# Optimization experiments

Measured on AMD Instinct MI355X. Metric: run time of the kernel, lower is better.

## Reference

```python
import jax, jax.numpy as jnp
import numpy as np
from jax import lax

B, S, D, T = 64, 256, 1024, 60
HIST = 20  # last-20 window of attn / decoder-state history


def setup_inputs() -> dict:
    key = jax.random.key(0)
    ks = jax.random.split(key, 8)
    e_outputs = jax.random.normal(ks[0], (B, S, D), jnp.float32)
    queries = jax.random.normal(ks[1], (B, T, D), jnp.float32)
    # attention weights over source frames: rows sum to 1
    attns = jax.nn.softmax(jax.random.normal(ks[2], (B, T, S), jnp.float32), axis=-1)
    g = 0.02
    Wr = jax.random.normal(ks[3], (D, 1), jnp.float32) * g
    br = jnp.zeros((1,), jnp.float32)
    Wa = jax.random.normal(ks[4], (D, 1), jnp.float32) * g
    ba = jnp.zeros((1,), jnp.float32)
    Wq = jax.random.normal(ks[5], (D, D), jnp.float32) / np.sqrt(D)
    Wn = jax.random.normal(ks[6], (2 * D, 1), jnp.float32) * g
    bn = jnp.zeros((1,), jnp.float32)
    return {"e_outputs": e_outputs, "queries": queries, "attns": attns,
            "Wr": Wr, "br": br, "Wa": Wa, "ba": ba, "Wq": Wq, "Wn": Wn, "bn": bn}


def reference(e_outputs, queries, attns, Wr, br, Wa, ba, Wq, Wn, bn):
    Bn, Sn, Dn = e_outputs.shape
    # decay1[i] = (i+1)/20 ; decay2[i] = 1-(i+1)/50, zero-padded past 50 frames
    decay1 = (jnp.arange(HIST, dtype=jnp.float32) + 1.0) / 20.0
    idx = jnp.arange(Sn, dtype=jnp.float32)
    add0 = jnp.where(idx < 50, 1.0 - (idx + 1.0) / 50.0, 0.0)
    add_state0 = add0[None, :, None]                       # [1,S,1]
    mem0 = e_outputs * add_state0                          # [B,S,D]
    abuf0 = jnp.zeros((HIST, Bn, Sn), e_outputs.dtype)
    qbuf0 = jnp.zeros((HIST, Bn, Dn), e_outputs.dtype)

    def step(carry, x):
        mem, add_state, abuf, qbuf, i = carry
        attn_i, q_i = x                                    # [B,S], [B,D]
        # read: selected frame before memory update
        sel = jnp.einsum('bs,bsd->bd', attn_i, mem)
        # roll history buffers (newest at slot HIST-1)
        abuf = jnp.concatenate([abuf[1:], attn_i[None]], axis=0)
        qbuf = jnp.concatenate([qbuf[1:], q_i[None]], axis=0)
        k = jnp.minimum(i + 1, HIST)
        valid = jnp.arange(HIST) >= (HIST - k)
        temp = jax.nn.softmax(jnp.where(valid, decay1, -jnp.inf))
        attn_w = jnp.einsum('t,tbs->bs', temp, abuf)       # decayed attn sum
        query_s = jnp.einsum('t,tbd->bd', temp, qbuf)      # decayed query sum
        remove_prob = jax.nn.sigmoid(q_i @ Wr + br)[:, :, None]   # [B,1,1]
        add_prob = jax.nn.sigmoid(q_i @ Wa + ba)[:, :, None]      # [B,1,1]
        sim = jax.nn.sigmoid(jnp.einsum('bsd,bd->bs', mem, query_s @ Wq))[..., None]
        mem = mem * (1.0 - remove_prob * attn_w[..., None] * sim)
        last_ctx = jnp.einsum('bs,bsd->bd', attn_w, e_outputs)[:, None, :]
        cat = jnp.concatenate([e_outputs, jnp.broadcast_to(last_ctx, e_outputs.shape)], axis=-1)
        nxt = jax.nn.sigmoid(cat @ Wn + bn)                # [B,S,1]
        mem = mem + e_outputs * (1.0 - add_state) * (add_prob * nxt)
        add_state = add_state + (1.0 - add_state) * (add_prob * nxt)
        return (mem, add_state, abuf, qbuf, i + 1), sel

    init = (mem0, jnp.broadcast_to(add_state0, (Bn, Sn, 1)), abuf0, qbuf0, jnp.int32(0))
    xs = (attns.transpose(1, 0, 2), queries.transpose(1, 0, 2))
    _, sels = lax.scan(step, init, xs)
    return sels.transpose(1, 0, 2)                         # [B,T,D]
```

## Files before the change

### kernel.cpp

```cpp
#include <hip/hip_runtime.h>
#include <math.h>


#define Bn 64
#define Sn 256
#define Dn 1024
#define Tn 60
#define HISTn 20
#define LDK 72
#define K05 1.0512710963760241f
#define EINV 0.36787944117144233f
#define LOG2E 1.4426950408889634f

typedef __bf16 bf16x8 __attribute__((ext_vector_type(8)));
typedef float f32x4 __attribute__((ext_vector_type(4)));
typedef unsigned short us8 __attribute__((ext_vector_type(8)));

typedef const __attribute__((address_space(1))) unsigned int* gas_u32p;
typedef __attribute__((address_space(3))) unsigned int* las_u32p;

__device__ __forceinline__ void gl16(const unsigned short* g, unsigned short* l){
  __builtin_amdgcn_global_load_lds((gas_u32p)g, (las_u32p)l, 16, 0, 0);
}

__device__ __forceinline__ unsigned short f2bf(float f){
  unsigned int x; __builtin_memcpy(&x,&f,4);
  unsigned int lsb = (x >> 16) & 1u;
  x += 0x7fffu + lsb;
  return (unsigned short)(x >> 16);
}
__device__ __forceinline__ float sigmoidf_(float x){
  float e = __builtin_amdgcn_exp2f(-x * LOG2E);
  return __builtin_amdgcn_rcpf(1.0f + e);
}

__global__ __launch_bounds__(256) void convQW(
    const float* __restrict__ Q, const float* __restrict__ Wr,
    const float* __restrict__ br, const float* __restrict__ Wa,
    const float* __restrict__ ba, const float* __restrict__ Wq,
    float* __restrict__ rp, float* __restrict__ ap,
    unsigned short* __restrict__ Qbf, unsigned short* __restrict__ WT)
{
  int tid = threadIdx.x;
  int bx = blockIdx.x;
  if (bx < Bn*Tn){
    int row = bx;
    float4 x = ((const float4*)(Q + (size_t)row*Dn))[tid];
    float4 a = ((const float4*)Wr)[tid];
    float4 b = ((const float4*)Wa)[tid];
    unsigned short o[4] = {f2bf(x.x), f2bf(x.y), f2bf(x.z), f2bf(x.w)};
    *(uint2*)&Qbf[(size_t)row*Dn + tid*4] = *(uint2*)o;
    float s1 = x.x*a.x + x.y*a.y + x.z*a.z + x.w*a.w;
    float s2 = x.x*b.x + x.y*b.y + x.z*b.z + x.w*b.w;
    for (int off = 32; off; off >>= 1){
      s1 += __shfl_down(s1, off, 64);
      s2 += __shfl_down(s2, off, 64);
    }
    __shared__ float r1[4], r2[4];
    int lane = tid & 63, wv = tid >> 6;
    if (lane == 0){ r1[wv] = s1; r2[wv] = s2; }
    __syncthreads();
    if (tid == 0){
      rp[row] = sigmoidf_(r1[0]+r1[1]+r1[2]+r1[3] + br[0]);
      ap[row] = sigmoidf_(r2[0]+r2[1]+r2[2]+r2[3] + ba[0]);
    }
  } else {
    __shared__ __align__(16) unsigned short Tt[64][LDK];
    int t = bx - Bn*Tn;
    int n0 = (t >> 4)*64, k0 = (t & 15)*64;
    int kl = tid >> 4, nl4 = (tid & 15)*4;
    #pragma unroll
    for (int it = 0; it < 4; it++){
      int k = kl + it*16;
      float4 v = *(const float4*)&Wq[(size_t)(k0+k)*Dn + n0 + nl4];
      Tt[nl4+0][k] = f2bf(v.x); Tt[nl4+1][k] = f2bf(v.y);
      Tt[nl4+2][k] = f2bf(v.z); Tt[nl4+3][k] = f2bf(v.w);
    }
    __syncthreads();
    int nr = tid >> 2, kg = (tid & 3)*16;
    *(us8*)&WT[(size_t)(n0+nr)*Dn + k0+kg]   = *(us8*)&Tt[nr][kg];
    *(us8*)&WT[(size_t)(n0+nr)*Dn + k0+kg+8] = *(us8*)&Tt[nr][kg+8];
  }
}

__global__ __launch_bounds__(256) void qw_e(
    const unsigned short* __restrict__ Qbf,
    const unsigned short* __restrict__ WT,
    const float* __restrict__ E, const float* __restrict__ Wn,
    unsigned short* __restrict__ QWbf,
    unsigned short* __restrict__ Ebf,
    float* __restrict__ eW1, float* __restrict__ eW2)
{
  int tid = threadIdx.x;
  if (blockIdx.x < (Bn*Tn/64)*(Dn/64)){
    __shared__ __align__(16) unsigned short As0_[64*64], Bs0_[64*64];
    __shared__ __align__(16) unsigned short As1_[64*64], Bs1_[64*64];
    int bx = (blockIdx.x & 7)*120 + (blockIdx.x >> 3);
    int m0 = (bx >> 4) * 64, n0 = (bx & 15) * 64;
    int lane = tid & 63, wave = tid >> 6;
    int quad = lane >> 4, l16 = lane & 15;
    f32x4 acc[4];
    #pragma unroll
    for (int nt=0;nt<4;nt++)
      #pragma unroll
      for (int r=0;r<4;r++) acc[nt][r]=0.f;
    int c0 = wave*2;
    int srow = c0*8 + (lane >> 3);
    int scol = ((lane & 7) ^ (lane >> 3)) * 8;
    const unsigned short* gA0 = Qbf + (size_t)(m0 + srow)*Dn + scol;
    const unsigned short* gA1 = gA0 + 8*Dn;
    const unsigned short* gB0 = WT  + (size_t)(n0 + srow)*Dn + scol;
    const unsigned short* gB1 = gB0 + 8*Dn;
    int mrow = wave*16 + l16;

    #define STAGE_QW(K, A_, B_) { \
      gl16(gA0 + (K), &A_[c0*512]);       \
      gl16(gA1 + (K), &A_[c0*512 + 512]); \
      gl16(gB0 + (K), &B_[c0*512]);       \
      gl16(gB1 + (K), &B_[c0*512 + 512]); }
    #define COMP_QW(A_, B_) { \
      _Pragma("unroll") \
      for (int kk = 0; kk < 2; kk++){ \
        bf16x8 a = *(const bf16x8*)&A_[ mrow*64 + ((kk*32 + quad*8) ^ ((mrow&7)*8)) ]; \
        _Pragma("unroll") \
        for (int nt=0;nt<4;nt++){ \
          int nrow = nt*16 + l16; \
          bf16x8 bb = *(const bf16x8*)&B_[ nrow*64 + ((kk*32 + quad*8) ^ ((nrow&7)*8)) ]; \
          acc[nt] = __builtin_amdgcn_mfma_f32_16x16x32_bf16(a, bb, acc[nt], 0, 0, 0); \
        } \
      } }

    STAGE_QW(0, As0_, Bs0_);
    __syncthreads();
    #pragma unroll
    for (int k0 = 0; k0 < Dn; k0 += 128){
      STAGE_QW(k0+64, As1_, Bs1_);
      COMP_QW(As0_, Bs0_);
      __syncthreads();
      if (k0+128 < Dn) STAGE_QW(k0+128, As0_, Bs0_);
      COMP_QW(As1_, Bs1_);
      __syncthreads();
    }
    #undef STAGE_QW
    #undef COMP_QW

    #pragma unroll
    for (int nt=0;nt<4;nt++)
      #pragma unroll
      for (int r=0;r<4;r++){
        int m = m0 + wave*16 + quad*4 + r;
        int n = n0 + nt*16 + l16;
        QWbf[(size_t)m*Dn + n] = f2bf(acc[nt][r]);
      }
  } else {
    int row = (blockIdx.x - (Bn*Tn/64)*(Dn/64))*4 + (tid >> 6);
    int lane = tid & 63;
    const float* er = E + (size_t)row*Dn;
    unsigned short* ebr = Ebf + (size_t)row*Dn;
    float d1 = 0.f, d2 = 0.f;
    #pragma unroll
    for (int c = 0; c < 4; c++){
      int idx = c*64 + lane;
      float4 v = ((const float4*)er)[idx];
      float4 w1 = ((const float4*)Wn)[idx];
      float4 w2 = ((const float4*)(Wn + Dn))[idx];
      unsigned short o[4] = {f2bf(v.x), f2bf(v.y), f2bf(v.z), f2bf(v.w)};
      ((uint2*)ebr)[idx] = *(uint2*)o;
      d1 += v.x*w1.x + v.y*w1.y + v.z*w1.z + v.w*w1.w;
      d2 += v.x*w2.x + v.y*w2.y + v.z*w2.z + v.w*w2.w;
    }
    #pragma unroll
    for (int off = 32; off; off >>= 1){
      d1 += __shfl_down(d1, off, 64);
      d2 += __shfl_down(d2, off, 64);
    }
    if (lane == 0){ eW1[row] = d1; eW2[row] = d2; }
  }
}

__global__ __launch_bounds__(256) void g_scan(
    const unsigned short* __restrict__ QWbf,
    const unsigned short* __restrict__ Ebf,
    const float* __restrict__ At,
    const float* __restrict__ rp,
    const float* __restrict__ ap,
    const float* __restrict__ eW1,
    const float* __restrict__ eW2,
    const float* __restrict__ bnp,
    unsigned short* __restrict__ Pbf)
{
  __shared__ __align__(16) unsigned short As0_[64][LDK], As1_[64][LDK];
  __shared__ __align__(16) unsigned short Bs0_[32][LDK], Bs1_[32][LDK];
  __shared__ __align__(16) float AtL[Tn][32], GL[Tn][32];
  __shared__ float Rsh[Tn], lcs[Tn], rps[Tn], aps[Tn], invd[Tn];
  int b = blockIdx.x, s0 = blockIdx.y * 32;
  int tid = threadIdx.x, lane = tid & 63, wave = tid >> 6;
  int quad = lane >> 4, l16 = lane & 15;

  {
    float4 e2v = ((const float4*)(eW2 + (size_t)b*Sn))[lane];
    const float* at_b = At + (size_t)b*Tn*Sn;
    #pragma unroll
    for (int w = 0; w < 15; w++){
      int j = wave + w*4;
      float4 a4 = ((const float4*)(at_b + (size_t)j*Sn))[lane];
      float v = a4.x*e2v.x + a4.y*e2v.y + a4.z*e2v.z + a4.w*e2v.w;
      #pragma unroll
      for (int off = 32; off; off >>= 1) v += __shfl_down(v, off, 64);
      if (lane == 0) Rsh[j] = v;
    }
  }
  {
    const float* at_c = At + (size_t)b*Tn*Sn + s0;
    #pragma unroll
    for (int it = 0; it < 2; it++){
      int idx = it*256 + tid;
      int r = idx >> 3, c4 = (idx & 7)*4;
      if (r < Tn) *(float4*)&AtL[r][c4] = *(const float4*)&at_c[(size_t)r*Sn + c4];
    }
  }
  if (tid < Tn){
    rps[tid] = rp[b*Tn + tid];
    aps[tid] = ap[b*Tn + tid];
  }

  f32x4 acc[2];
  #pragma unroll
  for (int nt=0;nt<2;nt++)
    #pragma unroll
    for (int r=0;r<4;r++) acc[nt][r]=0.f;
  int sr = tid >> 2, sk = (tid & 3)*16;
  int brw = tid >> 3, bk = (tid & 7)*8;
  const unsigned short* aRow = QWbf + ((size_t)(b*Tn + sr))*Dn;
  const unsigned short* bRow = Ebf  + ((size_t)(b*Sn + s0 + brw))*Dn;

  #define LOADR(K, ra0, ra1, rb0) { \
    if (sr < Tn){ ra0 = *(const us8*)&aRow[(K)+sk]; ra1 = *(const us8*)&aRow[(K)+sk+8]; } \
    else { ra0 = (us8)0; ra1 = (us8)0; } \
    rb0 = *(const us8*)&bRow[(K)+bk]; }
  #define STORER(A_, B_, ra0, ra1, rb0) { \
    *(us8*)&A_[sr][sk]   = ra0; *(us8*)&A_[sr][sk+8] = ra1; \
    *(us8*)&B_[brw][bk]  = rb0; }
  #define COMP_G(A_, B_) { \
    _Pragma("unroll") \
    for (int kk = 0; kk < 64; kk += 32){ \
      bf16x8 a = *(const bf16x8*)&A_[wave*16 + l16][kk + quad*8]; \
      _Pragma("unroll") \
      for (int nt=0;nt<2;nt++){ \
        bf16x8 bb = *(const bf16x8*)&B_[nt*16 + l16][kk + quad*8]; \
        acc[nt] = __builtin_amdgcn_mfma_f32_16x16x32_bf16(a, bb, acc[nt], 0, 0, 0); \
      } \
    } }

  us8 pa0, pa1, pb0, qa0, qa1, qb0;
  LOADR(0, pa0, pa1, pb0);
  STORER(As0_, Bs0_, pa0, pa1, pb0);
  for (int k0 = 0; k0 < Dn; k0 += 128){
    LOADR(k0+64, qa0, qa1, qb0);
    __syncthreads();
    COMP_G(As0_, Bs0_);
    STORER(As1_, Bs1_, qa0, qa1, qb0);
    if (k0+128 < Dn) LOADR(k0+128, pa0, pa1, pb0);
    __syncthreads();
    COMP_G(As1_, Bs1_);
    if (k0+128 < Dn) STORER(As0_, Bs0_, pa0, pa1, pb0);
  }
  #undef LOADR
  #undef STORER
  #undef COMP_G

  #pragma unroll
  for (int nt=0;nt<2;nt++)
    #pragma unroll
    for (int r=0;r<4;r++){
      int t = wave*16 + quad*4 + r;
      if (t < Tn) GL[t][nt*16 + l16] = acc[nt][r];
    }
  __syncthreads();

  if (tid < Tn){
    int i = tid;
    int j0 = (i - HISTn + 1 > 0) ? i - HISTn + 1 : 0;
    float num = 0.f, den = 0.f, wj = 1.f;
    #pragma unroll 1
    for (int j = 0; j <= i; j++){
      wj *= K05;
      if (j >= j0){ num += wj * Rsh[j]; den += wj; }
    }
    float inv = __builtin_amdgcn_rcpf(den);
    lcs[i] = num * inv;
    invd[i] = inv;
  }
  __syncthreads();

  if (tid < 32){
    int s = s0 + tid;
    float M = (s < 50) ? (1.0f - (s+1)/50.0f) : 0.0f;
    float A = M;
    float bnv = bnp[0];
    float e1 = eW1[b*Sn + s];
    unsigned short* P_b = Pbf + (size_t)b*Tn*Sn + s;
    float num_a = 0.f, num_q = 0.f, wi = 1.f;
    float a_new = AtL[0][tid], g_new = GL[0][tid];
    #pragma unroll 1
    for (int i = 0; i < Tn; i++){
      float a_nx = 0.f, g_nx = 0.f;
      if (i+1 < Tn){ a_nx = AtL[i+1][tid]; g_nx = GL[i+1][tid]; }
      wi *= K05;
      num_a += wi * a_new;
      num_q += wi * g_new;
      if (i >= HISTn){
        float wo = wi * EINV;
        num_a -= wo * AtL[i-HISTn][tid];
        num_q -= wo * GL[i-HISTn][tid];
      }
      float inv = invd[i];
      float aw = num_a * inv;
      float qd = num_q * inv;
      *P_b = f2bf(a_new * M);
      float sim = sigmoidf_(M * qd);
      float nxt = sigmoidf_(e1 + lcs[i] + bnv);
      M = M * (1.0f - rps[i] * aw * sim);
      float g = (1.0f - A) * aps[i] * nxt;
      M += g; A += g;
      a_new = a_nx; g_new = g_nx;
      P_b += Sn;
    }
  }
}

__global__ __launch_bounds__(256) void gemm_sels(
    const unsigned short* __restrict__ Pbf,
    const unsigned short* __restrict__ Ebf,
    float* __restrict__ out)
{
  __shared__ __align__(16) unsigned short As_[64][LDK], Bs_[64][LDK];
  int b = blockIdx.x, n0 = blockIdx.y*64;
  int tid = threadIdx.x, lane = tid & 63, wave = tid >> 6;
  int quad = lane >> 4, l16 = lane & 15;
  f32x4 acc[4];
  #pragma unroll
  for (int nt=0;nt<4;nt++)
    #pragma unroll
    for (int r=0;r<4;r++) acc[nt][r]=0.f;
  int sr = tid >> 2, sk = (tid & 3)*16;

  #define SLOAD(K) { \
    if (sr < Tn){ \
      const unsigned short* pp = &Pbf[((size_t)(b*Tn + sr))*Sn + (K)+sk]; \
      pa0 = *(const us8*)pp; pa1 = *(const us8*)(pp+8); \
    } else { pa0 = (us8)0; pa1 = (us8)0; } \
    const unsigned short* ep = &Ebf[((size_t)(b*Sn + (K) + sr))*Dn + n0 + sk]; \
    pe0 = *(const us8*)ep; pe1 = *(const us8*)(ep + 8); }
  #define SSTORE() { \
    *(us8*)&As_[sr][sk]   = pa0; *(us8*)&As_[sr][sk+8] = pa1; \
    _Pragma("unroll") \
    for (int j=0;j<8;j++){ \
      Bs_[sk+j][sr]   = pe0[j]; \
      Bs_[sk+8+j][sr] = pe1[j]; } }
  #define COMP_S() { \
    _Pragma("unroll") \
    for (int kk = 0; kk < 64; kk += 32){ \
      bf16x8 a = *(const bf16x8*)&As_[wave*16 + l16][kk + quad*8]; \
      _Pragma("unroll") \
      for (int nt=0;nt<4;nt++){ \
        bf16x8 bb = *(const bf16x8*)&Bs_[nt*16 + l16][kk + quad*8]; \
        acc[nt] = __builtin_amdgcn_mfma_f32_16x16x32_bf16(a, bb, acc[nt], 0, 0, 0); \
      } \
    } }

  us8 pa0, pa1, pe0, pe1;
  SLOAD(0);
  SSTORE();
  #pragma unroll
  for (int k0 = 0; k0 < Sn; k0 += 64){
    __syncthreads();
    if (k0+64 < Sn) SLOAD(k0+64);
    COMP_S();
    __syncthreads();
    if (k0+64 < Sn) SSTORE();
  }
  #undef SLOAD
  #undef SSTORE
  #undef COMP_S

  #pragma unroll
  for (int nt=0;nt<4;nt++)
    #pragma unroll
    for (int r=0;r<4;r++){
      int t = wave*16 + quad*4 + r;
      int d = n0 + nt*16 + l16;
      if (t < Tn) out[((size_t)(b*Tn + t))*Dn + d] = acc[nt][r];
    }
}

extern "C" void kernel_launch(void* const* d_in, const int* in_sizes, int n_in,
                              void* d_out, int out_size, void* d_ws, size_t ws_size,
                              hipStream_t stream)
{
  const float* E  = (const float*)d_in[0];
  const float* Q  = (const float*)d_in[1];
  const float* At = (const float*)d_in[2];
  const float* Wr = (const float*)d_in[3];
  const float* br = (const float*)d_in[4];
  const float* Wa = (const float*)d_in[5];
  const float* ba = (const float*)d_in[6];
  const float* Wq = (const float*)d_in[7];
  const float* Wn = (const float*)d_in[8];
  const float* bnp= (const float*)d_in[9];

  char* ws = (char*)d_ws;
  float* rp  = (float*)ws; ws += (size_t)Bn*Tn*4;
  float* ap  = (float*)ws; ws += (size_t)Bn*Tn*4;
  float* eW1 = (float*)ws; ws += (size_t)Bn*Sn*4;
  float* eW2 = (float*)ws; ws += (size_t)Bn*Sn*4;
  unsigned short* Qbf  = (unsigned short*)ws; ws += (size_t)Bn*Tn*Dn*2;
  unsigned short* WT   = (unsigned short*)ws; ws += (size_t)Dn*Dn*2;
  unsigned short* QWbf = (unsigned short*)ws; ws += (size_t)Bn*Tn*Dn*2;
  unsigned short* Ebf  = (unsigned short*)ws; ws += (size_t)Bn*Sn*Dn*2;
  unsigned short* Pbf = (unsigned short*)ws; ws += (size_t)Bn*Tn*Sn*2;

  convQW<<<Bn*Tn + 256, 256, 0, stream>>>(
      Q, Wr, br, Wa, ba, Wq, rp, ap, Qbf, WT);
  qw_e<<<(Bn*Tn/64)*(Dn/64) + Bn*Sn/4, 256, 0, stream>>>(
      Qbf, WT, E, Wn, QWbf, Ebf, eW1, eW2);
  g_scan<<<dim3(Bn, Sn/32), 256, 0, stream>>>(
      QWbf, Ebf, At, rp, ap, eW1, eW2, bnp, Pbf);
  gemm_sels<<<dim3(Bn, Dn/64), 256, 0, stream>>>(Pbf, Ebf, (float*)d_out);
}
```

Before: 191.2 us.

## Split fused G-GEMM/scan kernel and enlarge QW GEMM tiles to 128x128

The QW GEMM moves from 64x64 tiles with one 16-row strip per wave to 128x128 tiles where each wave computes a 64x64 sub-tile, raising register-level reuse and cutting the block count. The fused g_scan kernel is split into two. gemm_g computes G with 64-wide S tiles and writes it to a new fp32 global buffer. scan_s then runs the serial time scan with all 256 threads, one per source position, reading attention and G straight from global memory. This removes the case where only 32 of 256 threads ran the serial scan after the GEMM, at the cost of an extra kernel launch and a global round trip for G. It also leaves fewer, larger blocks for the QW GEMM.

```diff
diff --git a/kernel.cpp b/kernel.cpp
--- a/kernel.cpp
+++ b/kernel.cpp
@@ -92,68 +92,80 @@
     float* __restrict__ eW1, float* __restrict__ eW2)
 {
   int tid = threadIdx.x;
-  if (blockIdx.x < (Bn*Tn/64)*(Dn/64)){
-    __shared__ __align__(16) unsigned short As0_[64*64], Bs0_[64*64];
-    __shared__ __align__(16) unsigned short As1_[64*64], Bs1_[64*64];
-    int bx = (blockIdx.x & 7)*120 + (blockIdx.x >> 3);
-    int m0 = (bx >> 4) * 64, n0 = (bx & 15) * 64;
+  if (blockIdx.x < 240){
+    __shared__ __align__(16) unsigned short As0_[128*64], Bs0_[128*64];
+    __shared__ __align__(16) unsigned short As1_[128*64], Bs1_[128*64];
+    int bx = (blockIdx.x & 7)*30 + (blockIdx.x >> 3);
+    int m0 = (bx >> 3)*128, n0 = (bx & 7)*128;
     int lane = tid & 63, wave = tid >> 6;
     int quad = lane >> 4, l16 = lane & 15;
-    f32x4 acc[4];
-    #pragma unroll
-    for (int nt=0;nt<4;nt++)
+    int wr = (wave >> 1)*64, wc = (wave & 1)*64;
+    f32x4 acc[4][4];
+    #pragma unroll
+    for (int mi=0;mi<4;mi++)
       #pragma unroll
-      for (int r=0;r<4;r++) acc[nt][r]=0.f;
-    int c0 = wave*2;
-    int srow = c0*8 + (lane >> 3);
-    int scol = ((lane & 7) ^ (lane >> 3)) * 8;
-    const unsigned short* gA0 = Qbf + (size_t)(m0 + srow)*Dn + scol;
-    const unsigned short* gA1 = gA0 + 8*Dn;
-    const unsigned short* gB0 = WT  + (size_t)(n0 + srow)*Dn + scol;
-    const unsigned short* gB1 = gB0 + 8*Dn;
-    int mrow = wave*16 + l16;
-
-    #define STAGE_QW(K, A_, B_) { \
-      gl16(gA0 + (K), &A_[c0*512]);       \
-      gl16(gA1 + (K), &A_[c0*512 + 512]); \
-      gl16(gB0 + (K), &B_[c0*512]);       \
-      gl16(gB1 + (K), &B_[c0*512 + 512]); }
-    #define COMP_QW(A_, B_) { \
+      for (int ni=0;ni<4;ni++)
+        #pragma unroll
+        for (int r=0;r<4;r++) acc[mi][ni][r]=0.f;
+    int lr = lane >> 3;
+    int scol = ((lane & 7) ^ lr)*8;
+    const unsigned short* gA = Qbf + (size_t)(m0 + lr)*Dn + scol;
+    const unsigned short* gB = WT  + (size_t)(n0 + lr)*Dn + scol;
+
+    #define STAGE128(K, A_, B_) { \
       _Pragma("unroll") \
-      for (int kk = 0; kk < 2; kk++){ \
-        bf16x8 a = *(const bf16x8*)&A_[ mrow*64 + ((kk*32 + quad*8) ^ ((mrow&7)*8)) ]; \
+      for (int i = 0; i < 4; i++){ \
+        int c = wave*4 + i; \
+        gl16(gA + (size_t)c*8*Dn + (K), &A_[c*512]); \
+        gl16(gB + (size_t)c*8*Dn + (K), &B_[c*512]); \
+      } }
+    #define COMP128(A_, B_) { \
+      _Pragma("unroll") \
+      for (int ks = 0; ks < 2; ks++){ \
+        bf16x8 af[4], bg[4]; \
         _Pragma("unroll") \
-        for (int nt=0;nt<4;nt++){ \
-          int nrow = nt*16 + l16; \
-          bf16x8 bb = *(const bf16x8*)&B_[ nrow*64 + ((kk*32 + quad*8) ^ ((nrow&7)*8)) ]; \
-          acc[nt] = __builtin_amdgcn_mfma_f32_16x16x32_bf16(a, bb, acc[nt], 0, 0, 0); \
+        for (int mi=0;mi<4;mi++){ \
+          int mrow = wr + mi*16 + l16; \
+          af[mi] = *(const bf16x8*)&A_[mrow*64 + ((ks*32 + quad*8) ^ ((mrow&7)*8))]; \
         } \
+        _Pragma("unroll") \
+        for (int ni=0;ni<4;ni++){ \
+          int nrow = wc + ni*16 + l16; \
+          bg[ni] = *(const bf16x8*)&B_[nrow*64 + ((ks*32 + quad*8) ^ ((nrow&7)*8))]; \
+        } \
+        _Pragma("unroll") \
+        for (int mi=0;mi<4;mi++) \
+          _Pragma("unroll") \
+          for (int ni=0;ni<4;ni++) \
+            acc[mi][ni] = __builtin_amdgcn_mfma_f32_16x16x32_bf16(af[mi], bg[ni], acc[mi][ni], 0, 0, 0); \
       } }
 
-    STAGE_QW(0, As0_, Bs0_);
-    __syncthreads();
-    #pragma unroll
+    STAGE128(0, As0_, Bs0_);
+    __syncthreads();
+    #pragma unroll 1
     for (int k0 = 0; k0 < Dn; k0 += 128){
-      STAGE_QW(k0+64, As1_, Bs1_);
-      COMP_QW(As0_, Bs0_);
+      STAGE128(k0+64, As1_, Bs1_);
+      COMP128(As0_, Bs0_);
       __syncthreads();
-      if (k0+128 < Dn) STAGE_QW(k0+128, As0_, Bs0_);
-      COMP_QW(As1_, Bs1_);
+      if (k0+128 < Dn) STAGE128(k0+128, As0_, Bs0_);
+      COMP128(As1_, Bs1_);
       __syncthreads();
     }
-    #undef STAGE_QW
-    #undef COMP_QW
-
-    #pragma unroll
-    for (int nt=0;nt<4;nt++)
+    #undef STAGE128
+    #undef COMP128
+
+    #pragma unroll
+    for (int mi=0;mi<4;mi++)
       #pragma unroll
-      for (int r=0;r<4;r++){
-        int m = m0 + wave*16 + quad*4 + r;
-        int n = n0 + nt*16 + l16;
-        QWbf[(size_t)m*Dn + n] = f2bf(acc[nt][r]);
-      }
+      for (int ni=0;ni<4;ni++)
+        #pragma unroll
+        for (int r=0;r<4;r++){
+          int m = m0 + wr + mi*16 + quad*4 + r;
+          int n = n0 + wc + ni*16 + l16;
+          QWbf[(size_t)m*Dn + n] = f2bf(acc[mi][ni][r]);
+        }
   } else {
-    int row = (blockIdx.x - (Bn*Tn/64)*(Dn/64))*4 + (tid >> 6);
+    int row = (blockIdx.x - 240)*4 + (tid >> 6);
     int lane = tid & 63;
     const float* er = E + (size_t)row*Dn;
     unsigned short* ebr = Ebf + (size_t)row*Dn;
@@ -178,9 +190,72 @@
   }
 }
 
-__global__ __launch_bounds__(256) void g_scan(
+__global__ __launch_bounds__(256) void gemm_g(
     const unsigned short* __restrict__ QWbf,
     const unsigned short* __restrict__ Ebf,
+    float* __restrict__ G)
+{
+  __shared__ __align__(16) unsigned short As0_[64][LDK], Bs0_[64][LDK];
+  __shared__ __align__(16) unsigned short As1_[64][LDK], Bs1_[64][LDK];
+  int b = blockIdx.x, s0 = blockIdx.y*64;
+  int tid = threadIdx.x, lane = tid & 63, wave = tid >> 6;
+  int quad = lane >> 4, l16 = lane & 15;
+  f32x4 acc[4];
+  #pragma unroll
+  for (int nt=0;nt<4;nt++)
+    #pragma unroll
+    for (int r=0;r<4;r++) acc[nt][r]=0.f;
+  int sr = tid >> 2, sk = (tid & 3)*16;
+  const unsigned short* aRow = QWbf + ((size_t)(b*Tn + sr))*Dn;
+  const unsigned short* bRow = Ebf  + ((size_t)(b*Sn + s0 + sr))*Dn;
+
+  #define LOADR(K, ra0, ra1, rb0, rb1) { \
+    if (sr < Tn){ ra0 = *(const us8*)&aRow[(K)+sk]; ra1 = *(const us8*)&aRow[(K)+sk+8]; } \
+    else { ra0 = (us8)0; ra1 = (us8)0; } \
+    rb0 = *(const us8*)&bRow[(K)+sk]; rb1 = *(const us8*)&bRow[(K)+sk+8]; }
+  #define STORER(A_, B_, ra0, ra1, rb0, rb1) { \
+    *(us8*)&A_[sr][sk]   = ra0; *(us8*)&A_[sr][sk+8] = ra1; \
+    *(us8*)&B_[sr][sk]   = rb0; *(us8*)&B_[sr][sk+8] = rb1; }
+  #define COMP_G(A_, B_) { \
+    _Pragma("unroll") \
+    for (int kk = 0; kk < 64; kk += 32){ \
+      bf16x8 a = *(const bf16x8*)&A_[wave*16 + l16][kk + quad*8]; \
+      _Pragma("unroll") \
+      for (int nt=0;nt<4;nt++){ \
+        bf16x8 bb = *(const bf16x8*)&B_[nt*16 + l16][kk + quad*8]; \
+        acc[nt] = __builtin_amdgcn_mfma_f32_16x16x32_bf16(a, bb, acc[nt], 0, 0, 0); \
+      } \
+    } }
+
+  us8 pa0, pa1, pb0, pb1, qa0, qa1, qb0, qb1;
+  LOADR(0, pa0, pa1, pb0, pb1);
+  STORER(As0_, Bs0_, pa0, pa1, pb0, pb1);
+  #pragma unroll 1
+  for (int k0 = 0; k0 < Dn; k0 += 128){
+    LOADR(k0+64, qa0, qa1, qb0, qb1);
+    __syncthreads();
+    COMP_G(As0_, Bs0_);
+    STORER(As1_, Bs1_, qa0, qa1, qb0, qb1);
+    if (k0+128 < Dn) LOADR(k0+128, pa0, pa1, pb0, pb1);
+    __syncthreads();
+    COMP_G(As1_, Bs1_);
+    if (k0+128 < Dn) STORER(As0_, Bs0_, pa0, pa1, pb0, pb1);
+  }
+  #undef LOADR
+  #undef STORER
+  #undef COMP_G
+
+  #pragma unroll
+  for (int nt=0;nt<4;nt++)
+    #pragma unroll
+    for (int r=0;r<4;r++){
+      int t = wave*16 + quad*4 + r;
+      if (t < Tn) G[((size_t)(b*Tn + t))*Sn + s0 + nt*16 + l16] = acc[nt][r];
+    }
+}
+
+__global__ __launch_bounds__(256) void scan_s(
+    const float* __restrict__ G,
     const float* __restrict__ At,
     const float* __restrict__ rp,
     const float* __restrict__ ap,
@@ -189,13 +264,9 @@
     const float* __restrict__ bnp,
     unsigned short* __restrict__ Pbf)
 {
-  __shared__ __align__(16) unsigned short As0_[64][LDK], As1_[64][LDK];
-  __shared__ __align__(16) unsigned short Bs0_[32][LDK], Bs1_[32][LDK];
-  __shared__ __align__(16) float AtL[Tn][32], GL[Tn][32];
   __shared__ float Rsh[Tn], lcs[Tn], rps[Tn], aps[Tn], invd[Tn];
-  int b = blockIdx.x, s0 = blockIdx.y * 32;
-  int tid = threadIdx.x, lane = tid & 63, wave = tid >> 6;
-  int quad = lane >> 4, l16 = lane & 15;
+  int b = blockIdx.x, tid = threadIdx.x;
+  int lane = tid & 63, wave = tid >> 6;
 
   {
     float4 e2v = ((const float4*)(eW2 + (size_t)b*Sn))[lane];
@@ -210,72 +281,10 @@
       if (lane == 0) Rsh[j] = v;
     }
   }
-  {
-    const float* at_c = At + (size_t)b*Tn*Sn + s0;
-    #pragma unroll
-    for (int it = 0; it < 2; it++){
-      int idx = it*256 + tid;
-      int r = idx >> 3, c4 = (idx & 7)*4;
-      if (r < Tn) *(float4*)&AtL[r][c4] = *(const float4*)&at_c[(size_t)r*Sn + c4];
-    }
-  }
   if (tid < Tn){
     rps[tid] = rp[b*Tn + tid];
     aps[tid] = ap[b*Tn + tid];
   }
-
-  f32x4 acc[2];
-  #pragma unroll
-  for (int nt=0;nt<2;nt++)
-    #pragma unroll
-    for (int r=0;r<4;r++) acc[nt][r]=0.f;
-  int sr = tid >> 2, sk = (tid & 3)*16;
-  int brw = tid >> 3, bk = (tid & 7)*8;
-  const unsigned short* aRow = QWbf + ((size_t)(b*Tn + sr))*Dn;
-  const unsigned short* bRow = Ebf  + ((size_t)(b*Sn + s0 + brw))*Dn;
-
-  #define LOADR(K, ra0, ra1, rb0) { \
-    if (sr < Tn){ ra0 = *(const us8*)&aRow[(K)+sk]; ra1 = *(const us8*)&aRow[(K)+sk+8]; } \
-    else { ra0 = (us8)0; ra1 = (us8)0; } \
-    rb0 = *(const us8*)&bRow[(K)+bk]; }
-  #define STORER(A_, B_, ra0, ra1, rb0) { \
-    *(us8*)&A_[sr][sk]   = ra0; *(us8*)&A_[sr][sk+8] = ra1; \
-    *(us8*)&B_[brw][bk]  = rb0; }
-  #define COMP_G(A_, B_) { \
-    _Pragma("unroll") \
-    for (int kk = 0; kk < 64; kk += 32){ \
-      bf16x8 a = *(const bf16x8*)&A_[wave*16 + l16][kk + quad*8]; \
-      _Pragma("unroll") \
-      for (int nt=0;nt<2;nt++){ \
-        bf16x8 bb = *(const bf16x8*)&B_[nt*16 + l16][kk + quad*8]; \
-        acc[nt] = __builtin_amdgcn_mfma_f32_16x16x32_bf16(a, bb, acc[nt], 0, 0, 0); \
-      } \
-    } }
-
-  us8 pa0, pa1, pb0, qa0, qa1, qb0;
-  LOADR(0, pa0, pa1, pb0);
-  STORER(As0_, Bs0_, pa0, pa1, pb0);
-  for (int k0 = 0; k0 < Dn; k0 += 128){
-    LOADR(k0+64, qa0, qa1, qb0);
-    __syncthreads();
-    COMP_G(As0_, Bs0_);
-    STORER(As1_, Bs1_, qa0, qa1, qb0);
-    if (k0+128 < Dn) LOADR(k0+128, pa0, pa1, pb0);
-    __syncthreads();
-    COMP_G(As1_, Bs1_);
-    if (k0+128 < Dn) STORER(As0_, Bs0_, pa0, pa1, pb0);
-  }
-  #undef LOADR
-  #undef STORER
-  #undef COMP_G
-
-  #pragma unroll
-  for (int nt=0;nt<2;nt++)
-    #pragma unroll
-    for (int r=0;r<4;r++){
-      int t = wave*16 + quad*4 + r;
-      if (t < Tn) GL[t][nt*16 + l16] = acc[nt][r];
-    }
   __syncthreads();
 
   if (tid < Tn){
@@ -293,26 +302,33 @@
   }
   __syncthreads();
 
-  if (tid < 32){
-    int s = s0 + tid;
+  {
+    int s = tid;
     float M = (s < 50) ? (1.0f - (s+1)/50.0f) : 0.0f;
     float A = M;
     float bnv = bnp[0];
     float e1 = eW1[b*Sn + s];
+    const float* at_c = At + (size_t)b*Tn*Sn + s;
+    const float* g_c  = G  + (size_t)b*Tn*Sn + s;
     unsigned short* P_b = Pbf + (size_t)b*Tn*Sn + s;
     float num_a = 0.f, num_q = 0.f, wi = 1.f;
-    float a_new = AtL[0][tid], g_new = GL[0][tid];
+    float a_new = at_c[0], g_new = g_c[0];
+    float a_old = 0.f, g_old = 0.f;
     #pragma unroll 1
     for (int i = 0; i < Tn; i++){
       float a_nx = 0.f, g_nx = 0.f;
-      if (i+1 < Tn){ a_nx = AtL[i+1][tid]; g_nx = GL[i+1][tid]; }
+      if (i+1 < Tn){ a_nx = at_c[(size_t)(i+1)*Sn]; g_nx = g_c[(size_t)(i+1)*Sn]; }
+      if (i >= HISTn-1 && i < Tn-1){
+        a_old = at_c[(size_t)(i+1-HISTn)*Sn];
+        g_old = g_c[(size_t)(i+1-HISTn)*Sn];
+      }
       wi *= K05;
       num_a += wi * a_new;
       num_q += wi * g_new;
       if (i >= HISTn){
         float wo = wi * EINV;
-        num_a -= wo * AtL[i-HISTn][tid];
-        num_q -= wo * GL[i-HISTn][tid];
+        num_a -= wo * a_old;
+        num_q -= wo * g_old;
       }
       float inv = invd[i];
       float aw = num_a * inv;
@@ -418,13 +434,14 @@
   unsigned short* WT   = (unsigned short*)ws; ws += (size_t)Dn*Dn*2;
   unsigned short* QWbf = (unsigned short*)ws; ws += (size_t)Bn*Tn*Dn*2;
   unsigned short* Ebf  = (unsigned short*)ws; ws += (size_t)Bn*Sn*Dn*2;
+  float* G = (float*)ws; ws += (size_t)Bn*Tn*Sn*4;
   unsigned short* Pbf = (unsigned short*)ws; ws += (size_t)Bn*Tn*Sn*2;
 
   convQW<<<Bn*Tn + 256, 256, 0, stream>>>(
       Q, Wr, br, Wa, ba, Wq, rp, ap, Qbf, WT);
-  qw_e<<<(Bn*Tn/64)*(Dn/64) + Bn*Sn/4, 256, 0, stream>>>(
+  qw_e<<<240 + Bn*Sn/4, 256, 0, stream>>>(
       Qbf, WT, E, Wn, QWbf, Ebf, eW1, eW2);
-  g_scan<<<dim3(Bn, Sn/32), 256, 0, stream>>>(
-      QWbf, Ebf, At, rp, ap, eW1, eW2, bnp, Pbf);
+  gemm_g<<<dim3(Bn, Sn/64), 256, 0, stream>>>(QWbf, Ebf, G);
+  scan_s<<<Bn, 256, 0, stream>>>(G, At, rp, ap, eW1, eW2, bnp, Pbf);
   gemm_sels<<<dim3(Bn, Dn/64), 256, 0, stream>>>(Pbf, Ebf, (float*)d_out);
 }
```

After: 207.4 us. +8.5%, slower.
